# Optimization experiments

Hardware: AMD Instinct MI355X
Metric: run time of the kernel (lower is better)

## Reference

```python
import jax, jax.numpy as jnp
import numpy as np

N_CHAN = 64
N_PTS = 2048
D_IN = 256
D_OUT = 256
N_FRAMES = 32  # config.n_frames; no_frames = N_FRAMES - 1


def setup_inputs() -> dict:
    key = jax.random.key(0)
    k1, k2, k3, k4, k5 = jax.random.split(key, 5)
    x = jax.random.normal(k1, (N_CHAN, N_PTS, D_IN), dtype=jnp.float32)
    t = jax.random.uniform(k2, (1, N_CHAN, 1), dtype=jnp.float32)
    model_idx = jax.random.randint(k3, (N_CHAN,), 0, N_CHAN)
    # per-channel weights, SIREN-style uniform init scale
    bound = 1.0 / np.sqrt(D_IN)
    W = jax.random.uniform(k4, (N_CHAN, D_IN, D_OUT), minval=-bound, maxval=bound, dtype=jnp.float32)
    B = jax.random.uniform(k5, (N_FRAMES, D_OUT), minval=-bound, maxval=bound, dtype=jnp.float32)
    return {"x": x, "t": t, "model_idx": model_idx, "W": W, "B": B}


def reference(x, t, model_idx, W, B):
    no_frames = N_FRAMES - 1
    # bias index per channel from the time coordinate: (t[0,:,0] * no_frames).long()
    bias_idx = (t[0, :, 0] * no_frames).astype(jnp.int32)  # [C]
    Wg = W[model_idx]          # [C, D_IN, D_OUT] gathered per-channel weights
    bg = B[bias_idx]           # [C, D_OUT] gathered per-channel biases
    # batched per-channel linear: x [C, N, D_IN] @ Wg [C, D_IN, D_OUT]
    out = jnp.einsum('cni,cio->cno', x, Wg) + bg[:, None, :]
    return out
```

## Files before the change

### kernel.cpp

```cpp
#include <hip/hip_runtime.h>


#define M_PTS 2048
#define K_DIM 256
#define N_DIM 256
#define BT_STRIDE 264
#define WT_BYTES ((size_t)64 * K_DIM * N_DIM * 2)

typedef float floatx4 __attribute__((ext_vector_type(4)));
typedef __bf16 bf16x4 __attribute__((ext_vector_type(4)));
typedef __bf16 bf16x8 __attribute__((ext_vector_type(8)));

__device__ __forceinline__ __bf16 cvt_bf16(float f) {
  unsigned u = __builtin_bit_cast(unsigned, f);
  unsigned r = (u + 0x7FFFu + ((u >> 16) & 1u)) >> 16;
  return __builtin_bit_cast(__bf16, (unsigned short)r);
}

__global__ __launch_bounds__(256) void wt_k(const float* __restrict__ W,
                                            const int* __restrict__ MI,
                                            __bf16* __restrict__ Wt) {
  __shared__ float tile[64][65];
  const int bid = blockIdx.x;
  const int c  = bid >> 4;
  const int kt = (bid >> 2) & 3;
  const int nt = bid & 3;
  const float* __restrict__ src =
      W + (size_t)MI[c] * (K_DIM * N_DIM) + (size_t)(kt * 64) * N_DIM + nt * 64;
  __bf16* __restrict__ dst =
      Wt + (size_t)c * (K_DIM * N_DIM) + (size_t)(nt * 64) * K_DIM + kt * 64;
  const int tid = threadIdx.x;
  {
    const int nl = tid & 63, kl0 = tid >> 6;
#pragma unroll
    for (int u = 0; u < 16; ++u)
      tile[kl0 + u * 4][nl] = src[(size_t)(kl0 + u * 4) * N_DIM + nl];
  }
  __syncthreads();
  {
    const int kl = tid & 63, nl0 = tid >> 6;
#pragma unroll
    for (int u = 0; u < 16; ++u)
      dst[(size_t)(nl0 + u * 4) * K_DIM + kl] = cvt_bf16(tile[kl][nl0 + u * 4]);
  }
}

__global__ __launch_bounds__(256) void gemm_k(const float* __restrict__ X,
                                              const float* __restrict__ T,
                                              const __bf16* __restrict__ Wt,
                                              const float* __restrict__ Bb,
                                              float* __restrict__ Out) {
  const int bid = blockIdx.x;
  const int c   = bid >> 5;
  const int mg  = (bid >> 1) & 15;
  const int nt  = bid & 1;
  const int n0  = nt * 128;
  const int m0  = mg * 128;

  const int tid  = threadIdx.x;
  const int lane = tid & 63;
  const int w    = tid >> 6;
  const int wm   = w & 1;
  const int wn   = w >> 1;
  const int r    = lane & 15;
  const int kg   = lane >> 4;

  const float*  __restrict__ Xc = X  + (size_t)c * (M_PTS * K_DIM);
  const __bf16* __restrict__ Wc = Wt + (size_t)c * (K_DIM * N_DIM);

  const float* xa[4];
  const __bf16* wb[4];
#pragma unroll
  for (int i = 0; i < 4; ++i)
    xa[i] = Xc + (size_t)(m0 + wm * 64 + i * 16 + r) * K_DIM + kg * 8;
#pragma unroll
  for (int j = 0; j < 4; ++j)
    wb[j] = Wc + (size_t)(n0 + wn * 64 + j * 16 + r) * K_DIM + kg * 8;

  int bidx = (int)(T[c] * 31.0f);
  bidx = bidx < 0 ? 0 : (bidx > 31 ? 31 : bidx);
  const float* __restrict__ brow = Bb + bidx * N_DIM + n0 + wn * 64;
  float bv[4];
#pragma unroll
  for (int j = 0; j < 4; ++j) bv[j] = brow[j * 16 + r];

  floatx4 acc[4][4] = {};

#pragma unroll 2
  for (int kt = 0; kt < 8; ++kt) {
    const int k0 = kt * 32;
    floatx4 f0[4], f1[4];
    bf16x8 b[4];
#pragma unroll
    for (int i = 0; i < 4; ++i) {
      f0[i] = *(const floatx4*)(xa[i] + k0);
      f1[i] = *(const floatx4*)(xa[i] + k0 + 4);
    }
#pragma unroll
    for (int j = 0; j < 4; ++j) b[j] = *(const bf16x8*)(wb[j] + k0);
    bf16x8 a[4];
#pragma unroll
    for (int i = 0; i < 4; ++i)
#pragma unroll
      for (int v = 0; v < 4; ++v) {
        a[i][v]     = cvt_bf16(f0[i][v]);
        a[i][v + 4] = cvt_bf16(f1[i][v]);
      }
#pragma unroll
    for (int i = 0; i < 4; ++i)
#pragma unroll
      for (int j = 0; j < 4; ++j)
        acc[i][j] = __builtin_amdgcn_mfma_f32_16x16x32_bf16(a[i], b[j], acc[i][j], 0, 0, 0);
  }

  float* __restrict__ Oc = Out + (size_t)c * (M_PTS * N_DIM);
#pragma unroll
  for (int i = 0; i < 4; ++i) {
#pragma unroll
    for (int j = 0; j < 4; ++j) {
      const int col = n0 + wn * 64 + j * 16 + r;
#pragma unroll
      for (int v = 0; v < 4; ++v) {
        const int row = m0 + wm * 64 + i * 16 + kg * 4 + v;
        Oc[(size_t)row * N_DIM + col] = acc[i][j][v] + bv[j];
      }
    }
  }
}

__global__ __launch_bounds__(256) void fused_k(
    const float* __restrict__ X, const float* __restrict__ T,
    const int* __restrict__ MI, const float* __restrict__ W,
    const float* __restrict__ Bb, float* __restrict__ Out) {
  __shared__ __bf16 As[128 * 32];
  __shared__ __bf16 Bt[128 * BT_STRIDE];

  const int bid = blockIdx.x;
  const int c   = bid >> 4;
  const int mg  = (bid >> 1) & 7;
  const int nt  = bid & 1;
  const int n0  = nt * 128;

  const float* __restrict__ Xc = X + (size_t)c * (M_PTS * K_DIM);
  const float* __restrict__ Wc = W + (size_t)MI[c] * (K_DIM * N_DIM);

  const int tid  = threadIdx.x;
  const int lane = tid & 63;
  const int w    = tid >> 6;
  const int wm   = w & 1;
  const int wn   = w >> 1;
  const int r    = lane & 15;
  const int kg   = lane >> 4;

  {
    const int n  = tid & 127;
    const int kq = tid >> 7;
    const float* __restrict__ src = Wc + (size_t)(kq * 128) * N_DIM + n0 + n;
    __bf16* __restrict__ dst = &Bt[n * BT_STRIDE + kq * 128];
#pragma unroll 4
    for (int u = 0; u < 32; ++u) {
      bf16x4 v;
      v.x = cvt_bf16(src[(size_t)(u * 4 + 0) * N_DIM]);
      v.y = cvt_bf16(src[(size_t)(u * 4 + 1) * N_DIM]);
      v.z = cvt_bf16(src[(size_t)(u * 4 + 2) * N_DIM]);
      v.w = cvt_bf16(src[(size_t)(u * 4 + 3) * N_DIM]);
      *(bf16x4*)&dst[u * 4] = v;
    }
  }

  const int sm  = tid >> 1;
  const int skh = (tid & 1) * 16;
  const float* __restrict__ xrow = Xc + skh;
  __bf16* __restrict__ adst = &As[sm * 32 + skh];

  int bidx = (int)(T[c] * 31.0f);
  bidx = bidx < 0 ? 0 : (bidx > 31 ? 31 : bidx);
  const float* __restrict__ brow = Bb + bidx * N_DIM + n0 + wn * 64;
  float bv[4];
#pragma unroll
  for (int j = 0; j < 4; ++j) bv[j] = brow[j * 16 + r];

  float* __restrict__ Oc = Out + (size_t)c * (M_PTS * N_DIM);

  for (int mt2 = 0; mt2 < 2; ++mt2) {
    const int m0 = mg * 256 + mt2 * 128;
    const float* __restrict__ xsrc = xrow + (size_t)(m0 + sm) * K_DIM;
    floatx4 acc[4][4] = {};

    for (int kt = 0; kt < 8; ++kt) {
      const int k0 = kt * 32;
      __syncthreads();
      {
        floatx4 f0 = *(const floatx4*)(xsrc + k0 + 0);
        floatx4 f1 = *(const floatx4*)(xsrc + k0 + 4);
        floatx4 f2 = *(const floatx4*)(xsrc + k0 + 8);
        floatx4 f3 = *(const floatx4*)(xsrc + k0 + 12);
        bf16x8 h0, h1;
#pragma unroll
        for (int v = 0; v < 4; ++v) {
          h0[v]     = cvt_bf16(f0[v]);
          h0[v + 4] = cvt_bf16(f1[v]);
          h1[v]     = cvt_bf16(f2[v]);
          h1[v + 4] = cvt_bf16(f3[v]);
        }
        *(bf16x8*)&adst[0] = h0;
        *(bf16x8*)&adst[8] = h1;
      }
      __syncthreads();

      bf16x8 a[4], b[4];
#pragma unroll
      for (int i = 0; i < 4; ++i)
        a[i] = *(const bf16x8*)&As[(wm * 64 + i * 16 + r) * 32 + kg * 8];
#pragma unroll
      for (int j = 0; j < 4; ++j)
        b[j] = *(const bf16x8*)&Bt[(wn * 64 + j * 16 + r) * BT_STRIDE + k0 + kg * 8];
#pragma unroll
      for (int i = 0; i < 4; ++i)
#pragma unroll
        for (int j = 0; j < 4; ++j)
          acc[i][j] = __builtin_amdgcn_mfma_f32_16x16x32_bf16(a[i], b[j], acc[i][j], 0, 0, 0);
    }

#pragma unroll
    for (int i = 0; i < 4; ++i) {
#pragma unroll
      for (int j = 0; j < 4; ++j) {
        const int col = n0 + wn * 64 + j * 16 + r;
#pragma unroll
        for (int v = 0; v < 4; ++v) {
          const int row = m0 + wm * 64 + i * 16 + kg * 4 + v;
          Oc[(size_t)row * N_DIM + col] = acc[i][j][v] + bv[j];
        }
      }
    }
  }
}

extern "C" void kernel_launch(void* const* d_in, const int* in_sizes, int n_in,
                              void* d_out, int out_size, void* d_ws, size_t ws_size,
                              hipStream_t stream) {
  const float* X   = (const float*)d_in[0];
  const float* T   = (const float*)d_in[1];
  const int* MI    = (const int*)d_in[2];
  const float* W   = (const float*)d_in[3];
  const float* Bb  = (const float*)d_in[4];
  float* Out       = (float*)d_out;

  if (ws_size >= WT_BYTES && d_ws != nullptr) {
    __bf16* Wt = (__bf16*)d_ws;
    wt_k<<<dim3(1024), dim3(256), 0, stream>>>(W, MI, Wt);
    gemm_k<<<dim3(2048), dim3(256), 0, stream>>>(X, T, Wt, Bb, Out);
  } else {
    fused_k<<<dim3(1024), dim3(256), 0, stream>>>(X, T, MI, W, Bb, Out);
  }
}
```

Measured before the change: 304.6 us.

## Stage X tiles through double-buffered LDS with async global_load_lds and swizzle

```diff
diff --git a/kernel.cpp b/kernel.cpp
--- a/kernel.cpp
+++ b/kernel.cpp
@@ -10,6 +10,9 @@
 typedef float floatx4 __attribute__((ext_vector_type(4)));
 typedef __bf16 bf16x4 __attribute__((ext_vector_type(4)));
 typedef __bf16 bf16x8 __attribute__((ext_vector_type(8)));
+
+typedef __attribute__((address_space(3))) void lds_void;
+typedef const __attribute__((address_space(1))) void gbl_void;
 
 __device__ __forceinline__ __bf16 cvt_bf16(float f) {
   unsigned u = __builtin_bit_cast(unsigned, f);
@@ -45,15 +48,18 @@
   }
 }
 
-__global__ __launch_bounds__(256) void gemm_k(const float* __restrict__ X,
-                                              const float* __restrict__ T,
-                                              const __bf16* __restrict__ Wt,
-                                              const float* __restrict__ Bb,
-                                              float* __restrict__ Out) {
+__global__ __launch_bounds__(256, 4) void gemm_k(const float* __restrict__ X,
+                                                 const float* __restrict__ T,
+                                                 const __bf16* __restrict__ Wt,
+                                                 const float* __restrict__ Bb,
+                                                 float* __restrict__ Out) {
+  __shared__ float As[2][128 * 32];
+
   const int bid = blockIdx.x;
-  const int c   = bid >> 5;
-  const int mg  = (bid >> 1) & 15;
-  const int nt  = bid & 1;
+  const int wg  = ((bid & 7) << 8) | (bid >> 3);
+  const int c   = wg >> 5;
+  const int mg  = (wg >> 1) & 15;
+  const int nt  = wg & 1;
   const int n0  = nt * 128;
   const int m0  = mg * 128;
 
@@ -68,11 +74,22 @@
   const float*  __restrict__ Xc = X  + (size_t)c * (M_PTS * K_DIM);
   const __bf16* __restrict__ Wc = Wt + (size_t)c * (K_DIM * N_DIM);
 
-  const float* xa[4];
-  const __bf16* wb[4];
-#pragma unroll
-  for (int i = 0; i < 4; ++i)
-    xa[i] = Xc + (size_t)(m0 + wm * 64 + i * 16 + r) * K_DIM + kg * 8;
+  const int l8 = lane >> 3;
+  const int lc = lane & 7;
+  const float* __restrict__ xbase =
+      Xc + (size_t)(m0 + w * 32 + l8) * K_DIM + ((lc ^ l8) << 2);
+  const int lbase = (w * 32 + l8) * 32 + lc * 4;
+
+#define STAGE(kt_, buf_)                                                      \
+  {                                                                           \
+    _Pragma("unroll") for (int u = 0; u < 4; ++u) {                           \
+      __builtin_amdgcn_global_load_lds(                                       \
+          (gbl_void*)(xbase + (size_t)u * 8 * K_DIM + (kt_) * 32),            \
+          (lds_void*)(&As[buf_][lbase + u * 256]), 16, 0, 0);                 \
+    }                                                                         \
+  }
+
+  const __bf16* __restrict__ wb[4];
 #pragma unroll
   for (int j = 0; j < 4; ++j)
     wb[j] = Wc + (size_t)(n0 + wn * 64 + j * 16 + r) * K_DIM + kg * 8;
@@ -86,31 +103,38 @@
 
   floatx4 acc[4][4] = {};
 
-#pragma unroll 2
+  STAGE(0, 0);
+  int cur = 0;
+
   for (int kt = 0; kt < 8; ++kt) {
-    const int k0 = kt * 32;
-    floatx4 f0[4], f1[4];
+    __syncthreads();
+    if (kt < 7) STAGE(kt + 1, cur ^ 1);
+
     bf16x8 b[4];
 #pragma unroll
+    for (int j = 0; j < 4; ++j) b[j] = *(const bf16x8*)(wb[j] + kt * 32);
+
+    bf16x8 a[4];
+#pragma unroll
     for (int i = 0; i < 4; ++i) {
-      f0[i] = *(const floatx4*)(xa[i] + k0);
-      f1[i] = *(const floatx4*)(xa[i] + k0 + 4);
-    }
-#pragma unroll
-    for (int j = 0; j < 4; ++j) b[j] = *(const bf16x8*)(wb[j] + k0);
-    bf16x8 a[4];
-#pragma unroll
-    for (int i = 0; i < 4; ++i)
+      const int row = wm * 64 + i * 16 + r;
+      const int p0  = ((kg * 32) ^ ((r & 7) << 4)) >> 2;
+      const floatx4 f0 = *(const floatx4*)&As[cur][row * 32 + p0];
+      const floatx4 f1 = *(const floatx4*)&As[cur][row * 32 + (p0 ^ 4)];
 #pragma unroll
       for (int v = 0; v < 4; ++v) {
-        a[i][v]     = cvt_bf16(f0[i][v]);
-        a[i][v + 4] = cvt_bf16(f1[i][v]);
-      }
+        a[i][v]     = cvt_bf16(f0[v]);
+        a[i][v + 4] = cvt_bf16(f1[v]);
+      }
+    }
+
 #pragma unroll
     for (int i = 0; i < 4; ++i)
 #pragma unroll
       for (int j = 0; j < 4; ++j)
         acc[i][j] = __builtin_amdgcn_mfma_f32_16x16x32_bf16(a[i], b[j], acc[i][j], 0, 0, 0);
+
+    cur ^= 1;
   }
 
   float* __restrict__ Oc = Out + (size_t)c * (M_PTS * N_DIM);
@@ -126,6 +150,7 @@
       }
     }
   }
+#undef STAGE
 }
 
 __global__ __launch_bounds__(256) void fused_k(
```

After: 274.3 us. -10.0%, faster.
